# Optimization experiments

Measured on AMD Instinct MI355X. Metric: run time of the kernel, lower is better.

## Reference

```python
import jax, jax.numpy as jnp
import numpy as np


def _seq_shifts(n, max_len):
    # alternating-sign powers of two: [1,-1,2,-2,4,-4,...] capped by max_len
    shifts = []
    i = 0
    while len(shifts) < n and 2 ** i < max_len:
        shifts.append(2 ** i)
        if len(shifts) < n:
            shifts.append(-(2 ** i))
        i += 1
    return shifts

SPATIAL_SHIFTS = _seq_shifts(12, 2048)   # [1,-1,2,-2,4,-4,8,-8,16,-16,32,-32]
TEMPORAL_SHIFTS = _seq_shifts(4, 1 << 30)  # [1,-1,2,-2]
EPS = 1e-6


def setup_inputs() -> dict:
    key = jax.random.key(0)
    ks = jax.random.split(key, 8)
    B, L, C, H, D = 1, 8192, 1024, 16, 64
    inner = H * D
    w = 1.0 / np.sqrt(C)
    x = jax.random.normal(ks[0], (B, L, C), jnp.float32)
    Wq = jax.random.normal(ks[1], (C, inner), jnp.float32) * w
    Wk = jax.random.normal(ks[2], (C, inner), jnp.float32) * w
    Wv = jax.random.normal(ks[3], (C, inner), jnp.float32) * w
    Wo = jax.random.normal(ks[4], (inner, C), jnp.float32) * w
    bq = jnp.zeros((inner,), jnp.float32)
    bk = jnp.zeros((inner,), jnp.float32)
    bv = jnp.zeros((inner,), jnp.float32)
    bo = jnp.zeros((C,), jnp.float32)
    qn_w = jnp.ones((inner,), jnp.float32)
    kn_w = jnp.ones((inner,), jnp.float32)
    # edge bias initialized per the module's __init__ formula
    eb = np.zeros((H, len(SPATIAL_SHIFTS) + len(TEMPORAL_SHIFTS)), np.float32)
    for i, s in enumerate(SPATIAL_SHIFTS):
        eb[:, i] = 0.1 * np.log1p(abs(s))
    for i, s in enumerate(TEMPORAL_SHIFTS):
        eb[:, len(SPATIAL_SHIFTS) + i] = 0.2 * np.log1p(abs(s))
    edge_bias = jnp.asarray(eb)
    return {"x": x, "Wq": Wq, "bq": bq, "Wk": Wk, "bk": bk, "Wv": Wv, "bv": bv,
            "qn_w": qn_w, "kn_w": kn_w, "edge_bias": edge_bias, "Wo": Wo, "bo": bo,
            "num_frames": 8}


def _rms(t, w):
    return t * jax.lax.rsqrt(jnp.mean(t * t, axis=-1, keepdims=True) + EPS) * w


def reference(x, Wq, bq, Wk, bk, Wv, bv, qn_w, kn_w, edge_bias, Wo, bo, num_frames):
    B, L, _ = x.shape
    T = int(num_frames)
    S = L // T
    H, n_shifts = edge_bias.shape
    D = Wq.shape[1] // H
    scale = D ** -0.5
    msg = _rms(x @ Wq + bq, qn_w).reshape(B, T, S, H, D)
    key = _rms(x @ Wk + bk, kn_w).reshape(B, T, S, H, D)
    v5 = (x @ Wv + bv).reshape(B, T, S, H, D)
    scores, vals = [], []
    for s in SPATIAL_SHIFTS:  # neighbor idx (i+s)%S along spatial axis == roll(-s)
        k_nb = jnp.roll(key, -s, axis=2)
        vals.append(jnp.roll(v5, -s, axis=2))
        scores.append(jnp.einsum('btshd,btshd->btsh', msg, k_nb) * scale)
    for t in TEMPORAL_SHIFTS:  # neighbor idx (f+t)%T along frame axis
        k_nb = jnp.roll(key, -t, axis=1)
        vals.append(jnp.roll(v5, -t, axis=1))
        scores.append(jnp.einsum('btshd,btshd->btsh', msg, k_nb) * scale)
    sc = jnp.stack(scores, axis=-1) + edge_bias  # [B,T,S,H,N]
    attn = jax.nn.softmax(sc, axis=-1)
    v_stack = jnp.stack(vals, axis=-1)  # [B,T,S,H,D,N]
    out = jnp.einsum('btshn,btshdn->btshd', attn, v_stack).reshape(B, L, H * D)
    return out @ Wo + bo
```

## Files before the change

### kernel.cpp

```cpp
#include <hip/hip_runtime.h>
#include <hip/hip_bf16.h>

typedef __bf16 bf16x8 __attribute__((ext_vector_type(8)));
typedef float f32x4 __attribute__((ext_vector_type(4)));
typedef unsigned short ushort8 __attribute__((ext_vector_type(8)));
typedef unsigned short ushort_t;

#define AS3(p) ((__attribute__((address_space(3))) void*)(p))
#define AS1(p) ((const __attribute__((address_space(1))) void*)(p))

constexpr int L = 8192;
constexpr int C = 1024;
constexpr int T = 8;
constexpr int S = 1024;

__device__ __forceinline__ float bf2f(ushort_t u) {
    return __uint_as_float(((unsigned)u) << 16);
}
__device__ __forceinline__ ushort_t f2bf(float f) {
    unsigned x = __float_as_uint(f);
    unsigned r = (x + 0x7fffu + ((x >> 16) & 1u)) >> 16;
    return (ushort_t)r;
}

__global__ __launch_bounds__(256) void cvt_kernel(const float* __restrict__ in,
                                                  ushort_t* __restrict__ out, int n8) {
    int i = blockIdx.x * 256 + threadIdx.x;
    if (i >= n8) return;
    const float4* p = (const float4*)in + (long)i * 2;
    float4 a = p[0], b = p[1];
    ushort8 o;
    o[0] = f2bf(a.x); o[1] = f2bf(a.y); o[2] = f2bf(a.z); o[3] = f2bf(a.w);
    o[4] = f2bf(b.x); o[5] = f2bf(b.y); o[6] = f2bf(b.z); o[7] = f2bf(b.w);
    ((ushort8*)out)[i] = o;
}

__global__ __launch_bounds__(256) void transpose4_kernel(
    const float* __restrict__ w0, const float* __restrict__ w1,
    const float* __restrict__ w2, const float* __restrict__ w3,
    ushort_t* __restrict__ o0, ushort_t* __restrict__ o1,
    ushort_t* __restrict__ o2, ushort_t* __restrict__ o3) {
    int z = blockIdx.z;
    const float* W = z == 0 ? w0 : z == 1 ? w1 : z == 2 ? w2 : w3;
    ushort_t* O    = z == 0 ? o0 : z == 1 ? o1 : z == 2 ? o2 : o3;
    __shared__ float tile[32][33];
    int tx = threadIdx.x & 31, ty = threadIdx.x >> 5;
    int bx = blockIdx.x * 32, by = blockIdx.y * 32;
#pragma unroll
    for (int i = 0; i < 32; i += 8)
        tile[ty + i][tx] = W[(long)(by + ty + i) * C + bx + tx];
    __syncthreads();
#pragma unroll
    for (int i = 0; i < 32; i += 8)
        O[(long)(bx + ty + i) * C + by + tx] = f2bf(tile[tx][ty + i]);
}

#define VMBAR6() asm volatile("s_waitcnt vmcnt(6)\ns_barrier" ::: "memory")
#define VMBAR0() asm volatile("s_waitcnt vmcnt(0)\ns_barrier" ::: "memory")

template <bool BF16_OUT>
__device__ __forceinline__ void gemm_body(const ushort_t* __restrict__ A,
                                          const ushort_t* __restrict__ Bt,
                                          const float* __restrict__ bias,
                                          void* __restrict__ Cv,
                                          int K, int N, int bx, int by) {
    __shared__ char lds[3 * 24576];
    const int tid = threadIdx.x;
    const int wave = tid >> 6, lane = tid & 63;
    const int wm = wave >> 1, wn = wave & 1;
    const long bm0 = (long)bx * 256, bn0 = (long)by * 128;
    const int KT = K >> 5;

    const char* Ab = (const char*)A;
    const char* Bb = (const char*)Bt;
    long aSrc[4], bSrc[2];
#pragma unroll
    for (int j = 0; j < 4; j++) {
        int cc = tid + j * 256;
        aSrc[j] = (bm0 + (cc >> 2)) * (long)(K * 2) + (cc & 3) * 16;
    }
#pragma unroll
    for (int j = 0; j < 2; j++) {
        int cc = tid + j * 256;
        bSrc[j] = (bn0 + (cc >> 2)) * (long)(K * 2) + (cc & 3) * 16;
    }
    const unsigned wOff = wave * 1024u;

#define STG(buf, it2)                                                          \
    do {                                                                       \
        const long kb_ = (long)(it2) * 64;                                     \
        char* bs_ = lds + (buf) * 24576;                                       \
        _Pragma("unroll") for (int j = 0; j < 4; j++)                          \
            __builtin_amdgcn_global_load_lds(AS1(Ab + aSrc[j] + kb_),          \
                AS3(bs_ + j * 4096 + wOff), 16, 0, 0);                         \
        _Pragma("unroll") for (int j = 0; j < 2; j++)                          \
            __builtin_amdgcn_global_load_lds(AS1(Bb + bSrc[j] + kb_),          \
                AS3(bs_ + 16384 + j * 4096 + wOff), 16, 0, 0);                 \
    } while (0)

    const unsigned rdA = (wm * 128 + (lane & 15)) * 64u + (lane >> 4) * 16u;
    const unsigned rdB = 16384u + (wn * 64 + (lane & 15)) * 64u + (lane >> 4) * 16u;

    f32x4 acc[8][4] = {};

    STG(0, 0);
    STG(1, 1);
    VMBAR6();

    int c = 0;
    for (int it = 0; it < KT; ++it) {
        const int c2 = (c >= 1) ? c - 1 : 2;
        if (it + 2 < KT) STG(c2, it + 2);

        const char* bs = lds + c * 24576;
        bf16x8 af[8], bfr[4];
#pragma unroll
        for (int q = 0; q < 8; q++)
            af[q] = *(const bf16x8*)(bs + rdA + q * 1024);
#pragma unroll
        for (int j = 0; j < 4; j++)
            bfr[j] = *(const bf16x8*)(bs + rdB + j * 1024);

        __builtin_amdgcn_s_setprio(1);
#pragma unroll
        for (int q = 0; q < 8; q++)
#pragma unroll
            for (int j = 0; j < 4; j++)
                acc[q][j] = __builtin_amdgcn_mfma_f32_16x16x32_bf16(af[q], bfr[j],
                                                                    acc[q][j], 0, 0, 0);
        __builtin_amdgcn_s_setprio(0);

        if (it + 2 < KT)      VMBAR6();
        else if (it + 1 < KT) VMBAR0();
        c = (c >= 2) ? 0 : c + 1;
    }

    const int r0 = (int)bm0 + wm * 128 + (lane >> 4) * 4;
    const int c0 = (int)bn0 + wn * 64 + (lane & 15);
#pragma unroll
    for (int j = 0; j < 4; j++) {
        const int col = c0 + j * 16;
        const float bia = bias[col];
#pragma unroll
        for (int q = 0; q < 8; q++) {
            const int row = r0 + q * 16;
#pragma unroll
            for (int r = 0; r < 4; r++) {
                float val = acc[q][j][r] + bia;
                if (BF16_OUT)
                    ((ushort_t*)Cv)[(long)(row + r) * N + col] = f2bf(val);
                else
                    ((float*)Cv)[(long)(row + r) * N + col] = val;
            }
        }
    }
#undef STG
}

__global__ __launch_bounds__(256, 2) void gemm_qkv_kernel(
    const ushort_t* __restrict__ xbf,
    const ushort_t* __restrict__ WqT, const ushort_t* __restrict__ WkT,
    const ushort_t* __restrict__ WvT,
    const float* __restrict__ bq, const float* __restrict__ bk,
    const float* __restrict__ bv,
    ushort_t* __restrict__ q, ushort_t* __restrict__ k, ushort_t* __restrict__ v) {
    const int z = blockIdx.z;
    const ushort_t* Bt = z == 0 ? WqT : z == 1 ? WkT : WvT;
    const float* bias  = z == 0 ? bq : z == 1 ? bk : bv;
    ushort_t* out      = z == 0 ? q : z == 1 ? k : v;
    gemm_body<true>(xbf, Bt, bias, out, C, C, blockIdx.x, blockIdx.y);
}

__global__ __launch_bounds__(256, 2) void gemm_o_kernel(
    const ushort_t* __restrict__ a, const ushort_t* __restrict__ WoT,
    const float* __restrict__ bo, float* __restrict__ outp) {
    gemm_body<false>(a, WoT, bo, outp, C, C, blockIdx.x, blockIdx.y);
}

__global__ __launch_bounds__(256) void rownorm_k_kernel(
    const ushort_t* __restrict__ k, float* __restrict__ rk) {
    const int wave = threadIdx.x >> 6, lane = threadIdx.x & 63;
    const int p = blockIdx.x * 4 + wave;
    const ushort8* kp = (const ushort8*)(k + (long)p * C + lane * 16);
    ushort8 ka = kp[0], kb = kp[1];
    float sk = 0.f;
#pragma unroll
    for (int j = 0; j < 8; j++) {
        float c2 = bf2f(ka[j]), d = bf2f(kb[j]);
        sk += c2 * c2 + d * d;
    }
#pragma unroll
    for (int m = 1; m < 64; m <<= 1) sk += __shfl_xor(sk, m);
    if (lane == 0) rk[p] = rsqrtf(sk * (1.0f / C) + 1e-6f);
}

__global__ __launch_bounds__(256) void attn_kernel(
    const ushort_t* __restrict__ qraw, const ushort_t* __restrict__ kraw,
    const ushort_t* __restrict__ vraw,
    const float* __restrict__ qn_w, const float* __restrict__ kn_w,
    const float* __restrict__ eb, const float* __restrict__ rkA,
    ushort_t* __restrict__ outp) {
    const int wave = threadIdx.x >> 6, lane = threadIdx.x & 63;
    const int bid = blockIdx.x;
    const int t = bid & 7;
    const int s = (bid >> 3) * 4 + wave;
    const int p = (t << 10) | s;
    const int h = lane >> 2;
    const int cb = lane * 16;

    float qf[16];
    {
        const ushort8* qp = (const ushort8*)(qraw + (long)p * C + cb);
        ushort8 a = qp[0], b = qp[1];
#pragma unroll
        for (int j = 0; j < 8; j++) { qf[j] = bf2f(a[j]); qf[8 + j] = bf2f(b[j]); }
    }
    float ss = 0.f;
#pragma unroll
    for (int j = 0; j < 16; j++) ss += qf[j] * qf[j];
#pragma unroll
    for (int m = 1; m < 64; m <<= 1) ss += __shfl_xor(ss, m);
    const float rq = rsqrtf(ss * (1.0f / C) + 1e-6f);
#pragma unroll
    for (int j = 0; j < 16; j++) qf[j] *= rq * qn_w[cb + j] * kn_w[cb + j];

    const int SHF[16] = {1, -1, 2, -2, 4, -4, 8, -8, 16, -16, 32, -32, 1, -1, 2, -2};
    int pp[16];
#pragma unroll
    for (int n = 0; n < 16; n++) {
        if (n < 12) pp[n] = (p & ~(S - 1)) | ((s + SHF[n]) & (S - 1));
        else        pp[n] = (((t + SHF[n]) & (T - 1)) << 10) | s;
    }

    float sc[16];
#pragma unroll
    for (int n = 0; n < 16; n++) {
        const ushort8* kp = (const ushort8*)(kraw + (long)pp[n] * C + cb);
        ushort8 a = kp[0], b = kp[1];
        float dot = 0.f;
#pragma unroll
        for (int j = 0; j < 8; j++) dot += qf[j] * bf2f(a[j]) + qf[8 + j] * bf2f(b[j]);
        dot += __shfl_xor(dot, 1);
        dot += __shfl_xor(dot, 2);
        sc[n] = dot * (rkA[pp[n]] * 0.125f) + eb[h * 16 + n];
    }

    float mx = sc[0];
#pragma unroll
    for (int n = 1; n < 16; n++) mx = fmaxf(mx, sc[n]);
    float wts[16], den = 0.f;
#pragma unroll
    for (int n = 0; n < 16; n++) { wts[n] = __expf(sc[n] - mx); den += wts[n]; }
    const float inv = 1.0f / den;

    float o[16] = {};
#pragma unroll
    for (int n = 0; n < 16; n++) {
        const ushort8* vp = (const ushort8*)(vraw + (long)pp[n] * C + cb);
        ushort8 a = vp[0], b = vp[1];
#pragma unroll
        for (int j = 0; j < 8; j++) {
            o[j]     += wts[n] * bf2f(a[j]);
            o[8 + j] += wts[n] * bf2f(b[j]);
        }
    }

    ushort8 oa, ob;
#pragma unroll
    for (int j = 0; j < 8; j++) { oa[j] = f2bf(o[j] * inv); ob[j] = f2bf(o[8 + j] * inv); }
    ushort8* op = (ushort8*)(outp + (long)p * C + cb);
    op[0] = oa;
    op[1] = ob;
}

extern "C" void kernel_launch(void* const* d_in, const int* in_sizes, int n_in,
                              void* d_out, int out_size, void* d_ws, size_t ws_size,
                              hipStream_t stream) {
    const float* x    = (const float*)d_in[0];
    const float* Wq   = (const float*)d_in[1];
    const float* bq   = (const float*)d_in[2];
    const float* Wk   = (const float*)d_in[3];
    const float* bk   = (const float*)d_in[4];
    const float* Wv   = (const float*)d_in[5];
    const float* bv   = (const float*)d_in[6];
    const float* qn_w = (const float*)d_in[7];
    const float* kn_w = (const float*)d_in[8];
    const float* eb   = (const float*)d_in[9];
    const float* Wo   = (const float*)d_in[10];
    const float* bo   = (const float*)d_in[11];

    char* ws = (char*)d_ws;
    ushort_t* xbf  = (ushort_t*)ws;
    ushort_t* WqT  = (ushort_t*)(ws + (size_t)L * C * 2);
    ushort_t* WkT  = WqT + (size_t)C * C;
    ushort_t* WvT  = WkT + (size_t)C * C;
    ushort_t* WoT  = WvT + (size_t)C * C;
    ushort_t* qraw = WoT + (size_t)C * C;
    ushort_t* kraw = qraw + (size_t)L * C;
    ushort_t* vraw = kraw + (size_t)L * C;
    ushort_t* aout = vraw + (size_t)L * C;
    float* rkArr   = (float*)(aout + (size_t)L * C);
    float* outp = (float*)d_out;

    cvt_kernel<<<(L * C / 8 + 255) / 256, 256, 0, stream>>>(x, xbf, L * C / 8);
    transpose4_kernel<<<dim3(32, 32, 4), 256, 0, stream>>>(Wq, Wk, Wv, Wo,
                                                           WqT, WkT, WvT, WoT);
    gemm_qkv_kernel<<<dim3(L / 256, C / 128, 3), 256, 0, stream>>>(
        xbf, WqT, WkT, WvT, bq, bk, bv, qraw, kraw, vraw);
    rownorm_k_kernel<<<L / 4, 256, 0, stream>>>(kraw, rkArr);
    attn_kernel<<<L / 4, 256, 0, stream>>>(qraw, kraw, vraw, qn_w, kn_w, eb,
                                           rkArr, aout);
    gemm_o_kernel<<<dim3(L / 256, C / 128), 256, 0, stream>>>(aout, WoT, bo, outp);
}
```

Before: 237.5 us.

## Use 256x256 GEMM tiles with swizzled LDS, head-major QKV, head-blocked attention

The GEMMs move to 256x256 tiles with 512 threads, a 4-slot LDS ring (128 KB) and an XOR swizzle on the 16-byte chunks so more K tiles are in flight with fewer bank conflicts. The QKV epilogue writes q/k/v in a head-major [H][L][64] layout. The rownorm kernel now computes both q and k inverse RMS. The attention kernel is regridded so each block handles one head and 32 spatial positions, with 8 lanes per position, which aims for better locality of neighbour K/V reads. Risks include lower occupancy from the large LDS footprint and scattered 2-byte stores in the head-major epilogue.

```diff
diff --git a/kernel.cpp b/kernel.cpp
--- a/kernel.cpp
+++ b/kernel.cpp
@@ -13,6 +13,7 @@
 constexpr int C = 1024;
 constexpr int T = 8;
 constexpr int S = 1024;
+constexpr int KT_C = 32;
 
 __device__ __forceinline__ float bf2f(ushort_t u) {
     return __uint_as_float(((unsigned)u) << 16);
@@ -55,71 +56,63 @@
         O[(long)(bx + ty + i) * C + by + tx] = f2bf(tile[tx][ty + i]);
 }
 
-#define VMBAR6() asm volatile("s_waitcnt vmcnt(6)\ns_barrier" ::: "memory")
-#define VMBAR0() asm volatile("s_waitcnt vmcnt(0)\ns_barrier" ::: "memory")
-
-template <bool BF16_OUT>
-__device__ __forceinline__ void gemm_body(const ushort_t* __restrict__ A,
-                                          const ushort_t* __restrict__ Bt,
-                                          const float* __restrict__ bias,
-                                          void* __restrict__ Cv,
-                                          int K, int N, int bx, int by) {
-    __shared__ char lds[3 * 24576];
+#define VMW(n) asm volatile("s_waitcnt vmcnt(" #n ")" ::: "memory")
+
+template <int OUT_MODE>
+__device__ __forceinline__ void gemm256_body(const ushort_t* __restrict__ A,
+                                             const ushort_t* __restrict__ Bt,
+                                             const float* __restrict__ bias,
+                                             void* __restrict__ Cv,
+                                             int bx, int by) {
+    __shared__ char lds[4 * 32768];
     const int tid = threadIdx.x;
     const int wave = tid >> 6, lane = tid & 63;
-    const int wm = wave >> 1, wn = wave & 1;
-    const long bm0 = (long)bx * 256, bn0 = (long)by * 128;
-    const int KT = K >> 5;
+    const int wm = wave >> 2, wn = wave & 3;
+    const long bm0 = (long)bx * 256, bn0 = (long)by * 256;
 
     const char* Ab = (const char*)A;
     const char* Bb = (const char*)Bt;
-    long aSrc[4], bSrc[2];
-#pragma unroll
-    for (int j = 0; j < 4; j++) {
-        int cc = tid + j * 256;
-        aSrc[j] = (bm0 + (cc >> 2)) * (long)(K * 2) + (cc & 3) * 16;
-    }
+    long aSrc[2], bSrc[2];
 #pragma unroll
     for (int j = 0; j < 2; j++) {
-        int cc = tid + j * 256;
-        bSrc[j] = (bn0 + (cc >> 2)) * (long)(K * 2) + (cc & 3) * 16;
-    }
-    const unsigned wOff = wave * 1024u;
-
-#define STG(buf, it2)                                                          \
-    do {                                                                       \
-        const long kb_ = (long)(it2) * 64;                                     \
-        char* bs_ = lds + (buf) * 24576;                                       \
-        _Pragma("unroll") for (int j = 0; j < 4; j++)                          \
-            __builtin_amdgcn_global_load_lds(AS1(Ab + aSrc[j] + kb_),          \
-                AS3(bs_ + j * 4096 + wOff), 16, 0, 0);                         \
-        _Pragma("unroll") for (int j = 0; j < 2; j++)                          \
-            __builtin_amdgcn_global_load_lds(AS1(Bb + bSrc[j] + kb_),          \
-                AS3(bs_ + 16384 + j * 4096 + wOff), 16, 0, 0);                 \
+        int c = tid + j * 512, row = c >> 2, scol = (c & 3) ^ ((row >> 1) & 3);
+        aSrc[j] = (bm0 + row) * (long)(C * 2) + scol * 16;
+        bSrc[j] = (bn0 + row) * (long)(C * 2) + scol * 16;
+    }
+    const unsigned dOff = wave * 1024u;
+
+#define STG(slot, it)                                                            \
+    do {                                                                         \
+        const long kb_ = (long)(it) * 64;                                        \
+        char* s_ = lds + (slot) * 32768;                                         \
+        __builtin_amdgcn_global_load_lds(AS1(Ab + aSrc[0] + kb_),                \
+                                         AS3(s_ + dOff), 16, 0, 0);              \
+        __builtin_amdgcn_global_load_lds(AS1(Ab + aSrc[1] + kb_),                \
+                                         AS3(s_ + 8192 + dOff), 16, 0, 0);       \
+        __builtin_amdgcn_global_load_lds(AS1(Bb + bSrc[0] + kb_),                \
+                                         AS3(s_ + 16384 + dOff), 16, 0, 0);      \
+        __builtin_amdgcn_global_load_lds(AS1(Bb + bSrc[1] + kb_),                \
+                                         AS3(s_ + 24576 + dOff), 16, 0, 0);      \
     } while (0)
 
-    const unsigned rdA = (wm * 128 + (lane & 15)) * 64u + (lane >> 4) * 16u;
-    const unsigned rdB = 16384u + (wn * 64 + (lane & 15)) * 64u + (lane >> 4) * 16u;
+    const unsigned sl = ((lane >> 4) ^ ((lane >> 1) & 3)) * 16u;
+    const unsigned rdA = (wm * 128 + (lane & 15)) * 64u + sl;
+    const unsigned rdB = 16384u + (wn * 64 + (lane & 15)) * 64u + sl;
 
     f32x4 acc[8][4] = {};
 
-    STG(0, 0);
-    STG(1, 1);
-    VMBAR6();
-
-    int c = 0;
-    for (int it = 0; it < KT; ++it) {
-        const int c2 = (c >= 1) ? c - 1 : 2;
-        if (it + 2 < KT) STG(c2, it + 2);
-
-        const char* bs = lds + c * 24576;
+    STG(0, 0); STG(1, 1); STG(2, 2);
+    VMW(8);
+    __builtin_amdgcn_s_barrier();
+
+    for (int it = 0; it < KT_C; ++it) {
+        if (it + 3 < KT_C) STG((it + 3) & 3, it + 3);
+        const char* bs = lds + (it & 3) * 32768;
         bf16x8 af[8], bfr[4];
 #pragma unroll
-        for (int q = 0; q < 8; q++)
-            af[q] = *(const bf16x8*)(bs + rdA + q * 1024);
-#pragma unroll
-        for (int j = 0; j < 4; j++)
-            bfr[j] = *(const bf16x8*)(bs + rdB + j * 1024);
+        for (int q = 0; q < 8; q++) af[q] = *(const bf16x8*)(bs + rdA + q * 1024);
+#pragma unroll
+        for (int j = 0; j < 4; j++) bfr[j] = *(const bf16x8*)(bs + rdB + j * 1024);
 
         __builtin_amdgcn_s_setprio(1);
 #pragma unroll
@@ -130,9 +123,10 @@
                                                                     acc[q][j], 0, 0, 0);
         __builtin_amdgcn_s_setprio(0);
 
-        if (it + 2 < KT)      VMBAR6();
-        else if (it + 1 < KT) VMBAR0();
-        c = (c >= 2) ? 0 : c + 1;
+        if (it + 3 < KT_C)      { VMW(8); }
+        else if (it + 2 < KT_C) { VMW(4); }
+        else if (it + 1 < KT_C) { VMW(0); }
+        if (it + 1 < KT_C) __builtin_amdgcn_s_barrier();
     }
 
     const int r0 = (int)bm0 + wm * 128 + (lane >> 4) * 4;
@@ -147,17 +141,18 @@
 #pragma unroll
             for (int r = 0; r < 4; r++) {
                 float val = acc[q][j][r] + bia;
-                if (BF16_OUT)
-                    ((ushort_t*)Cv)[(long)(row + r) * N + col] = f2bf(val);
+                if (OUT_MODE == 1)
+                    ((ushort_t*)Cv)[(size_t)(col >> 6) * (L * 64) +
+                                    (long)(row + r) * 64 + (col & 63)] = f2bf(val);
                 else
-                    ((float*)Cv)[(long)(row + r) * N + col] = val;
+                    ((float*)Cv)[(long)(row + r) * C + col] = val;
             }
         }
     }
 #undef STG
 }
 
-__global__ __launch_bounds__(256, 2) void gemm_qkv_kernel(
+__global__ __launch_bounds__(512, 2) void gemm_qkv_kernel(
     const ushort_t* __restrict__ xbf,
     const ushort_t* __restrict__ WqT, const ushort_t* __restrict__ WkT,
     const ushort_t* __restrict__ WvT,
@@ -168,80 +163,85 @@
     const ushort_t* Bt = z == 0 ? WqT : z == 1 ? WkT : WvT;
     const float* bias  = z == 0 ? bq : z == 1 ? bk : bv;
     ushort_t* out      = z == 0 ? q : z == 1 ? k : v;
-    gemm_body<true>(xbf, Bt, bias, out, C, C, blockIdx.x, blockIdx.y);
-}
-
-__global__ __launch_bounds__(256, 2) void gemm_o_kernel(
+    gemm256_body<1>(xbf, Bt, bias, out, blockIdx.x, blockIdx.y);
+}
+
+__global__ __launch_bounds__(512, 2) void gemm_o_kernel(
     const ushort_t* __restrict__ a, const ushort_t* __restrict__ WoT,
     const float* __restrict__ bo, float* __restrict__ outp) {
-    gemm_body<false>(a, WoT, bo, outp, C, C, blockIdx.x, blockIdx.y);
-}
-
-__global__ __launch_bounds__(256) void rownorm_k_kernel(
-    const ushort_t* __restrict__ k, float* __restrict__ rk) {
+    gemm256_body<0>(a, WoT, bo, outp, blockIdx.x, blockIdx.y);
+}
+
+__global__ __launch_bounds__(256) void rownorm_kernel(
+    const ushort_t* __restrict__ q, const ushort_t* __restrict__ k,
+    float* __restrict__ rq, float* __restrict__ rk) {
     const int wave = threadIdx.x >> 6, lane = threadIdx.x & 63;
     const int p = blockIdx.x * 4 + wave;
-    const ushort8* kp = (const ushort8*)(k + (long)p * C + lane * 16);
-    ushort8 ka = kp[0], kb = kp[1];
-    float sk = 0.f;
+    const int h = lane >> 2, qt = lane & 3;
+    const size_t base = (size_t)h * (L * 64) + (long)p * 64 + qt * 16;
+    const ushort8* qp = (const ushort8*)(q + base);
+    const ushort8* kp = (const ushort8*)(k + base);
+    ushort8 qa = qp[0], qb = qp[1], ka = kp[0], kb = kp[1];
+    float sq = 0.f, sk = 0.f;
 #pragma unroll
     for (int j = 0; j < 8; j++) {
+        float a = bf2f(qa[j]), b = bf2f(qb[j]);
+        sq += a * a + b * b;
         float c2 = bf2f(ka[j]), d = bf2f(kb[j]);
         sk += c2 * c2 + d * d;
     }
 #pragma unroll
-    for (int m = 1; m < 64; m <<= 1) sk += __shfl_xor(sk, m);
-    if (lane == 0) rk[p] = rsqrtf(sk * (1.0f / C) + 1e-6f);
+    for (int m = 1; m < 64; m <<= 1) { sq += __shfl_xor(sq, m); sk += __shfl_xor(sk, m); }
+    if (lane == 0) {
+        rq[p] = rsqrtf(sq * (1.0f / C) + 1e-6f);
+        rk[p] = rsqrtf(sk * (1.0f / C) + 1e-6f);
+    }
 }
 
 __global__ __launch_bounds__(256) void attn_kernel(
     const ushort_t* __restrict__ qraw, const ushort_t* __restrict__ kraw,
     const ushort_t* __restrict__ vraw,
     const float* __restrict__ qn_w, const float* __restrict__ kn_w,
-    const float* __restrict__ eb, const float* __restrict__ rkA,
-    ushort_t* __restrict__ outp) {
+    const float* __restrict__ eb, const float* __restrict__ rqA,
+    const float* __restrict__ rkA, ushort_t* __restrict__ outp) {
+    const int bid = blockIdx.x;
+    const int t = bid & 7, chunk = (bid >> 3) & 31, h = bid >> 8;
     const int wave = threadIdx.x >> 6, lane = threadIdx.x & 63;
-    const int bid = blockIdx.x;
-    const int t = bid & 7;
-    const int s = (bid >> 3) * 4 + wave;
+    const int pos = lane >> 3, cg = lane & 7;
+    const int s = chunk * 32 + wave * 8 + pos;
     const int p = (t << 10) | s;
-    const int h = lane >> 2;
-    const int cb = lane * 16;
-
-    float qf[16];
+
+    const ushort_t* qb = qraw + (size_t)h * (L * 64);
+    const ushort_t* kb = kraw + (size_t)h * (L * 64);
+    const ushort_t* vb = vraw + (size_t)h * (L * 64);
+
+    float qf[8];
     {
-        const ushort8* qp = (const ushort8*)(qraw + (long)p * C + cb);
-        ushort8 a = qp[0], b = qp[1];
-#pragma unroll
-        for (int j = 0; j < 8; j++) { qf[j] = bf2f(a[j]); qf[8 + j] = bf2f(b[j]); }
-    }
-    float ss = 0.f;
-#pragma unroll
-    for (int j = 0; j < 16; j++) ss += qf[j] * qf[j];
-#pragma unroll
-    for (int m = 1; m < 64; m <<= 1) ss += __shfl_xor(ss, m);
-    const float rq = rsqrtf(ss * (1.0f / C) + 1e-6f);
-#pragma unroll
-    for (int j = 0; j < 16; j++) qf[j] *= rq * qn_w[cb + j] * kn_w[cb + j];
+        ushort8 qv = *(const ushort8*)(qb + (long)p * 64 + cg * 8);
+        const float rqv = rqA[p];
+#pragma unroll
+        for (int j = 0; j < 8; j++)
+            qf[j] = bf2f(qv[j]) * rqv * qn_w[h * 64 + cg * 8 + j] * kn_w[h * 64 + cg * 8 + j];
+    }
 
     const int SHF[16] = {1, -1, 2, -2, 4, -4, 8, -8, 16, -16, 32, -32, 1, -1, 2, -2};
     int pp[16];
 #pragma unroll
     for (int n = 0; n < 16; n++) {
-        if (n < 12) pp[n] = (p & ~(S - 1)) | ((s + SHF[n]) & (S - 1));
+        if (n < 12) pp[n] = (t << 10) | ((s + SHF[n]) & (S - 1));
         else        pp[n] = (((t + SHF[n]) & (T - 1)) << 10) | s;
     }
 
     float sc[16];
 #pragma unroll
     for (int n = 0; n < 16; n++) {
-        const ushort8* kp = (const ushort8*)(kraw + (long)pp[n] * C + cb);
-        ushort8 a = kp[0], b = kp[1];
+        ushort8 kv = *(const ushort8*)(kb + (long)pp[n] * 64 + cg * 8);
         float dot = 0.f;
 #pragma unroll
-        for (int j = 0; j < 8; j++) dot += qf[j] * bf2f(a[j]) + qf[8 + j] * bf2f(b[j]);
+        for (int j = 0; j < 8; j++) dot += qf[j] * bf2f(kv[j]);
         dot += __shfl_xor(dot, 1);
         dot += __shfl_xor(dot, 2);
+        dot += __shfl_xor(dot, 4);
         sc[n] = dot * (rkA[pp[n]] * 0.125f) + eb[h * 16 + n];
     }
 
@@ -253,24 +253,18 @@
     for (int n = 0; n < 16; n++) { wts[n] = __expf(sc[n] - mx); den += wts[n]; }
     const float inv = 1.0f / den;
 
-    float o[16] = {};
+    float o[8] = {};
 #pragma unroll
     for (int n = 0; n < 16; n++) {
-        const ushort8* vp = (const ushort8*)(vraw + (long)pp[n] * C + cb);
-        ushort8 a = vp[0], b = vp[1];
-#pragma unroll
-        for (int j = 0; j < 8; j++) {
-            o[j]     += wts[n] * bf2f(a[j]);
-            o[8 + j] += wts[n] * bf2f(b[j]);
-        }
-    }
-
-    ushort8 oa, ob;
-#pragma unroll
-    for (int j = 0; j < 8; j++) { oa[j] = f2bf(o[j] * inv); ob[j] = f2bf(o[8 + j] * inv); }
-    ushort8* op = (ushort8*)(outp + (long)p * C + cb);
-    op[0] = oa;
-    op[1] = ob;
+        ushort8 vv = *(const ushort8*)(vb + (long)pp[n] * 64 + cg * 8);
+#pragma unroll
+        for (int j = 0; j < 8; j++) o[j] += wts[n] * bf2f(vv[j]);
+    }
+
+    ushort8 ov;
+#pragma unroll
+    for (int j = 0; j < 8; j++) ov[j] = f2bf(o[j] * inv);
+    *(ushort8*)(outp + (long)p * C + h * 64 + cg * 8) = ov;
 }
 
 extern "C" void kernel_launch(void* const* d_in, const int* in_sizes, int n_in,
@@ -299,16 +293,17 @@
     ushort_t* kraw = qraw + (size_t)L * C;
     ushort_t* vraw = kraw + (size_t)L * C;
     ushort_t* aout = vraw + (size_t)L * C;
-    float* rkArr   = (float*)(aout + (size_t)L * C);
+    float* rqArr   = (float*)(aout + (size_t)L * C);
+    float* rkArr   = rqArr + L;
     float* outp = (float*)d_out;
 
     cvt_kernel<<<(L * C / 8 + 255) / 256, 256, 0, stream>>>(x, xbf, L * C / 8);
     transpose4_kernel<<<dim3(32, 32, 4), 256, 0, stream>>>(Wq, Wk, Wv, Wo,
                                                            WqT, WkT, WvT, WoT);
-    gemm_qkv_kernel<<<dim3(L / 256, C / 128, 3), 256, 0, stream>>>(
+    gemm_qkv_kernel<<<dim3(L / 256, C / 256, 3), 512, 0, stream>>>(
         xbf, WqT, WkT, WvT, bq, bk, bv, qraw, kraw, vraw);
-    rownorm_k_kernel<<<L / 4, 256, 0, stream>>>(kraw, rkArr);
-    attn_kernel<<<L / 4, 256, 0, stream>>>(qraw, kraw, vraw, qn_w, kn_w, eb,
-                                           rkArr, aout);
-    gemm_o_kernel<<<dim3(L / 256, C / 128), 256, 0, stream>>>(aout, WoT, bo, outp);
-}
+    rownorm_kernel<<<L / 4, 256, 0, stream>>>(qraw, kraw, rqArr, rkArr);
+    attn_kernel<<<T * 32 * 16, 256, 0, stream>>>(qraw, kraw, vraw, qn_w, kn_w, eb,
+                                                 rqArr, rkArr, aout);
+    gemm_o_kernel<<<dim3(L / 256, C / 256), 512, 0, stream>>>(aout, WoT, bo, outp);
+}
```

Result: slower. 276.4 us (+16.4%).
